# Kernel tuning notes

Measured on AMD Instinct MI355X. Metric: run time of the kernel, lower is better.

The kernel has to match this reference:

```python
import jax, jax.numpy as jnp
import numpy as np
import math

B, H, T, N = 2, 16, 4096, 64  # N = mlp_internal_dim_multiplier * n_embd // n_head = 1*1024//16
THETA = 2.0 ** 16


def _cos_sin(T, N):
    # quantized-theta RoPE tables, matching get_freqs + angle construction
    t = jnp.arange(N, dtype=jnp.float32)
    tq = jnp.floor(t / 2.0) * 2.0                      # quantize(t, q=2)
    freqs = 1.0 / (THETA ** (tq / N)) / (2.0 * math.pi)  # [N]
    phases = jnp.arange(T, dtype=jnp.float32)[:, None] * freqs[None, :]  # [T,N]
    ang = (phases % 1.0) * (2.0 * math.pi)
    return jnp.cos(ang), jnp.sin(ang)                  # each [T,N]


def setup_inputs() -> dict:
    key = jax.random.key(0)
    kq, kv = jax.random.split(key)
    Q = jax.random.normal(kq, (B, H, T, N), dtype=jnp.float32)
    V = jax.random.normal(kv, (B, H, T, N), dtype=jnp.float32)
    return {"Q": Q, "V": V}


def reference(Q, V):
    # K is Q (asserted in the torch module); RoPE applied to Q only.
    b, h, t, n = Q.shape
    cos, sin = _cos_sin(t, n)                          # [t,n], broadcast over b,h
    q_rot = jnp.stack((-Q[..., 1::2], Q[..., ::2]), axis=-1).reshape(Q.shape)
    QR = Q * cos + q_rot * sin                         # [b,h,t,n]
    scores = jnp.einsum('bhtn,bhsn->bhts', QR, QR) * (n ** -0.5)
    # strict lower-triangular mask (tril with diagonal=-1): no softmax
    mask = jnp.tril(jnp.ones((t, t), dtype=bool), k=-1)
    scores = jnp.where(mask, scores, 0.0)
    return jnp.einsum('bhts,bhsn->bhtn', scores, V)
```

## Files before the change

kernel.cpp:

```cpp
#include <hip/hip_runtime.h>

#define T_SEQ 4096
#define NDIM 64
#define BH 32
#define TN (T_SEQ * NDIM)

typedef short short8 __attribute__((ext_vector_type(8)));
typedef float f32x16 __attribute__((ext_vector_type(16)));

static __device__ __forceinline__ unsigned short f2bf(float x) {
    union { float f; unsigned u; } v; v.f = x;
    return (unsigned short)((v.u + 0x8000u) >> 16);
}

static __device__ __forceinline__ f32x16 mfma32(short8 a, short8 b, f32x16 c) {
    return __builtin_amdgcn_mfma_f32_32x32x16_bf16(a, b, c, 0, 0, 0);
}


__global__ __launch_bounds__(256) void rope_kernel(const float* __restrict__ Q,
                                                   unsigned short* __restrict__ qf) {
    const int bhtb = blockIdx.x;
    const int tb = bhtb & 127;
    const int bh = bhtb >> 7;
    const int np = threadIdx.x & 31;
    const int tg = threadIdx.x >> 5;
    const float freq = exp2f(-0.5f * (float)np) * 0.15915494309189535f;
    const int kc = np >> 3, hi = (np >> 2) & 1, jw = np & 3;
    const float2* qsrc = (const float2*)(Q + ((size_t)bh * T_SEQ + tb * 32) * NDIM);
    unsigned* qdst = (unsigned*)(qf + (size_t)bh * TN + (size_t)tb * 32 * NDIM);
#pragma unroll
    for (int it = 0; it < 4; ++it) {
        const int tl = tg * 4 + it;
        const int t = tb * 32 + tl;
        float2 q = qsrc[tl * 32 + np];
        float ph = (float)t * freq;
        float ang = (ph - floorf(ph)) * 6.283185307179586f;
        float s, c;
        __sincosf(ang, &s, &c);
        float r0 = q.x * c - q.y * s;
        float r1 = q.y * c + q.x * s;
        unsigned pk = (unsigned)f2bf(r0) | ((unsigned)f2bf(r1) << 16);
        qdst[kc * 256 + (tl * 2 + hi) * 4 + jw] = pk;
    }
}

__global__ __launch_bounds__(256) void vtrans_kernel(const float* __restrict__ V,
                                                     unsigned short* __restrict__ vfr) {
    __shared__ float tile[128 * 65];
    const int sb = blockIdx.x;
    const int bh = blockIdx.y;
    const int tid = threadIdx.x;
    const float* vsrc = V + ((size_t)bh * T_SEQ + sb * 128) * NDIM;
#pragma unroll
    for (int i = 0; i < 8; ++i) {
        int e = (i * 256 + tid) * 4;
        int row = e >> 6, col = e & 63;
        float4 d4 = *(const float4*)(vsrc + e);
        tile[row * 65 + col + 0] = d4.x; tile[row * 65 + col + 1] = d4.y;
        tile[row * 65 + col + 2] = d4.z; tile[row * 65 + col + 3] = d4.w;
    }
    __syncthreads();
    unsigned short* dst = vfr + (size_t)bh * TN + (size_t)sb * 8192;
#pragma unroll
    for (int u = 0; u < 4; ++u) {
        int g = u * 256 + tid;
        int kc = g >> 7, dh = g & 127;
        int d = dh >> 1, hh = dh & 1;
        int sbase = kc * 16 + hh * 8;
        ushort4 o0, o1;
        o0.x = f2bf(tile[(sbase + 0) * 65 + d] * 0.125f);
        o0.y = f2bf(tile[(sbase + 1) * 65 + d] * 0.125f);
        o0.z = f2bf(tile[(sbase + 2) * 65 + d] * 0.125f);
        o0.w = f2bf(tile[(sbase + 3) * 65 + d] * 0.125f);
        o1.x = f2bf(tile[(sbase + 4) * 65 + d] * 0.125f);
        o1.y = f2bf(tile[(sbase + 5) * 65 + d] * 0.125f);
        o1.z = f2bf(tile[(sbase + 6) * 65 + d] * 0.125f);
        o1.w = f2bf(tile[(sbase + 7) * 65 + d] * 0.125f);
        *(ushort4*)(dst + g * 8 + 0) = o0;
        *(ushort4*)(dst + g * 8 + 4) = o1;
    }
}

#define LDP 136

__global__ __launch_bounds__(256, 2) void attn_kernel(const unsigned short* __restrict__ qf,
                                                      const unsigned short* __restrict__ vfr,
                                                      float* __restrict__ out) {
    __shared__ unsigned short ps[128 * LDP];

    const int tid = threadIdx.x;
    const int lane = tid & 63;
    const int w = tid >> 6;
    const int ws = w >> 1, wt = w & 1;
    const int l31 = lane & 31, hi = lane >> 5;
    const int swz = (l31 & 8);

    const int blk = blockIdx.x;
    const int bh = blk & 31;
    const int qb = 31 - (blk >> 5);
    const int t0 = qb * 128;

    const unsigned short* qfh = qf + (size_t)bh * TN;
    const unsigned short* vfh = vfr + (size_t)bh * TN;
    float* out_h = out + (size_t)bh * TN;

    const int lhx16 = (l31 * 2 + hi) * 8;

    short8 bq[2][4];
#pragma unroll
    for (int tt2 = 0; tt2 < 2; ++tt2) {
        const int r32 = (t0 >> 5) + 2 * wt + tt2;
#pragma unroll
        for (int kc = 0; kc < 4; ++kc)
            bq[tt2][kc] = *(const short8*)(qfh + (size_t)(r32 * 4 + kc) * 512 + lhx16);
    }

    f32x16 oacc[2];
#pragma unroll
    for (int m = 0; m < 2; ++m)
#pragma unroll
        for (int r = 0; r < 16; ++r) oacc[m][r] = 0.0f;

    short8 ak[2][4];
#pragma unroll
    for (int st2 = 0; st2 < 2; ++st2) {
        const int r32 = 2 * ws + st2;
#pragma unroll
        for (int kc = 0; kc < 4; ++kc)
            ak[st2][kc] = *(const short8*)(qfh + (size_t)(r32 * 4 + kc) * 512 + lhx16);
    }

    for (int sb = 0; sb <= qb; ++sb) {
        short8 vf[8];
#pragma unroll
        for (int kc = 0; kc < 8; ++kc)
            vf[kc] = *(const short8*)(vfh + (size_t)sb * 8192 + (size_t)kc * 1024 +
                                      (size_t)wt * 512 + lhx16);

        f32x16 sacc[2][2];
#pragma unroll
        for (int a = 0; a < 2; ++a)
#pragma unroll
            for (int b = 0; b < 2; ++b)
#pragma unroll
                for (int r = 0; r < 16; ++r) sacc[a][b][r] = 0.0f;
#pragma unroll
        for (int st2 = 0; st2 < 2; ++st2)
#pragma unroll
            for (int tt2 = 0; tt2 < 2; ++tt2)
#pragma unroll
                for (int kc = 0; kc < 4; ++kc)
                    sacc[st2][tt2] = mfma32(ak[st2][kc], bq[tt2][kc], sacc[st2][tt2]);

        short8 akn[2][4];
        if (sb < qb) {
#pragma unroll
            for (int st2 = 0; st2 < 2; ++st2) {
                const int r32 = ((sb + 1) * 4) + 2 * ws + st2;
#pragma unroll
                for (int kc = 0; kc < 4; ++kc)
                    akn[st2][kc] = *(const short8*)(qfh + (size_t)(r32 * 4 + kc) * 512 + lhx16);
            }
        }

        __syncthreads();

        const bool diag = (sb == qb);
#pragma unroll
        for (int st2 = 0; st2 < 2; ++st2) {
            const int st = 2 * ws + st2;
#pragma unroll
            for (int tt2 = 0; tt2 < 2; ++tt2) {
                const int trow = (2 * wt + tt2) * 32 + l31;
                unsigned short* pbase = &ps[trow * LDP + st * 32 + 4 * hi + swz];
                if (!diag) {
#pragma unroll
                    for (int g = 0; g < 4; ++g) {
                        ushort4 pk;
                        pk.x = f2bf(sacc[st2][tt2][4 * g + 0]);
                        pk.y = f2bf(sacc[st2][tt2][4 * g + 1]);
                        pk.z = f2bf(sacc[st2][tt2][4 * g + 2]);
                        pk.w = f2bf(sacc[st2][tt2][4 * g + 3]);
                        *(ushort4*)(pbase + 8 * g) = pk;
                    }
                } else {
#pragma unroll
                    for (int g = 0; g < 4; ++g) {
                        ushort4 pk;
#pragma unroll
                        for (int e = 0; e < 4; ++e) {
                            const int srow = st * 32 + 8 * g + 4 * hi + e;
                            float v = sacc[st2][tt2][4 * g + e];
                            if (srow >= trow) v = 0.0f;
                            ((unsigned short*)&pk)[e] = f2bf(v);
                        }
                        *(ushort4*)(pbase + 8 * g) = pk;
                    }
                }
            }
        }
        __syncthreads();

#pragma unroll
        for (int kc = 0; kc < 8; ++kc) {
            short8 pf0 = *(const short8*)&ps[((2 * ws + 0) * 32 + l31) * LDP +
                                             kc * 16 + hi * 8 + swz];
            short8 pf1 = *(const short8*)&ps[((2 * ws + 1) * 32 + l31) * LDP +
                                             kc * 16 + hi * 8 + swz];
            oacc[0] = mfma32(pf0, vf[kc], oacc[0]);
            oacc[1] = mfma32(pf1, vf[kc], oacc[1]);
        }

        if (sb < qb) {
#pragma unroll
            for (int st2 = 0; st2 < 2; ++st2)
#pragma unroll
                for (int kc = 0; kc < 4; ++kc)
                    ak[st2][kc] = akn[st2][kc];
        }
    }

#pragma unroll
    for (int mt2 = 0; mt2 < 2; ++mt2) {
        const int mt = 2 * ws + mt2;
#pragma unroll
        for (int r = 0; r < 16; ++r) {
            const int rl = (r & 3) + 8 * (r >> 2) + 4 * hi;
            out_h[(size_t)(t0 + mt * 32 + rl) * NDIM + wt * 32 + l31] = oacc[mt2][r];
        }
    }
}

extern "C" void kernel_launch(void* const* d_in, const int* in_sizes, int n_in,
                              void* d_out, int out_size, void* d_ws, size_t ws_size,
                              hipStream_t stream) {
    (void)in_sizes; (void)n_in; (void)out_size; (void)ws_size;
    const float* Q = (const float*)d_in[0];
    const float* V = (const float*)d_in[1];
    float* out = (float*)d_out;

    unsigned short* qf  = (unsigned short*)d_ws;
    unsigned short* vfr = qf + (size_t)BH * TN;

    rope_kernel<<<BH * 128, 256, 0, stream>>>(Q, qf);
    vtrans_kernel<<<dim3(T_SEQ / 128, BH), 256, 0, stream>>>(V, vfr);
    attn_kernel<<<BH * 32, 256, 0, stream>>>(qf, vfr, out);
}
```

Measured before the change: 181.0 us.

## Keep score tiles in registers via permlane swap instead of LDS round-trip

The attention inner loop no longer writes bf16 score tiles to shared memory and reads them back with two barriers per block. The score accumulator is converted in registers into MFMA A-operand fragments using a cross-half lane swap (permlane32_swap or a bpermute fallback). The work split changes so each wave pair covers a slice of the key dimension and produces partial outputs. These partials are reduced once through LDS at the end. This removes per-iteration LDS traffic and synchronization, at the cost of more accumulator registers and a final cross-wave reduction.

```diff
diff --git a/kernel.cpp b/kernel.cpp
--- a/kernel.cpp
+++ b/kernel.cpp
@@ -7,16 +7,50 @@
 
 typedef short short8 __attribute__((ext_vector_type(8)));
 typedef float f32x16 __attribute__((ext_vector_type(16)));
+typedef unsigned uint2e __attribute__((ext_vector_type(2)));
 
 static __device__ __forceinline__ unsigned short f2bf(float x) {
     union { float f; unsigned u; } v; v.f = x;
     return (unsigned short)((v.u + 0x8000u) >> 16);
 }
-
+static __device__ __forceinline__ unsigned packbf(float lo, float hi) {
+    return (unsigned)f2bf(lo) | ((unsigned)f2bf(hi) << 16);
+}
 static __device__ __forceinline__ f32x16 mfma32(short8 a, short8 b, f32x16 c) {
     return __builtin_amdgcn_mfma_f32_32x32x16_bf16(a, b, c, 0, 0, 0);
 }
 
+static __device__ __forceinline__ void half_swap(unsigned &x, unsigned &y) {
+#if __has_builtin(__builtin_amdgcn_permlane32_swap)
+    uint2e r = __builtin_amdgcn_permlane32_swap(x, y, false, false);
+    x = r[0]; y = r[1];
+#else
+    int sl = (((int)threadIdx.x & 63) ^ 32) << 2;
+    unsigned bx = (unsigned)__builtin_amdgcn_ds_bpermute(sl, (int)x);
+    unsigned by = (unsigned)__builtin_amdgcn_ds_bpermute(sl, (int)y);
+    bool hi = (threadIdx.x & 32) != 0;
+    unsigned nx = hi ? by : x;
+    unsigned ny = hi ? y : bx;
+    x = nx; y = ny;
+#endif
+}
+
+static __device__ __forceinline__ void tile_to_frags(const f32x16 &sc, short8 &f0, short8 &f1) {
+    unsigned d[4][2];
+#pragma unroll
+    for (int g = 0; g < 4; ++g) {
+        d[g][0] = packbf(sc[4 * g + 0], sc[4 * g + 1]);
+        d[g][1] = packbf(sc[4 * g + 2], sc[4 * g + 3]);
+    }
+    half_swap(d[0][0], d[1][0]);
+    half_swap(d[0][1], d[1][1]);
+    half_swap(d[2][0], d[3][0]);
+    half_swap(d[2][1], d[3][1]);
+    union { unsigned u[4]; short8 s; } a, b;
+    a.u[0] = d[0][0]; a.u[1] = d[0][1]; a.u[2] = d[1][0]; a.u[3] = d[1][1];
+    b.u[0] = d[2][0]; b.u[1] = d[2][1]; b.u[2] = d[3][0]; b.u[3] = d[3][1];
+    f0 = a.s; f1 = b.s;
+}
 
 __global__ __launch_bounds__(256) void rope_kernel(const float* __restrict__ Q,
                                                    unsigned short* __restrict__ qf) {
@@ -82,19 +116,16 @@
     }
 }
 
-#define LDP 136
-
 __global__ __launch_bounds__(256, 2) void attn_kernel(const unsigned short* __restrict__ qf,
                                                       const unsigned short* __restrict__ vfr,
                                                       float* __restrict__ out) {
-    __shared__ unsigned short ps[128 * LDP];
+    __shared__ float4 red[2][4][4][64];
 
     const int tid = threadIdx.x;
     const int lane = tid & 63;
     const int w = tid >> 6;
     const int ws = w >> 1, wt = w & 1;
     const int l31 = lane & 31, hi = lane >> 5;
-    const int swz = (l31 & 8);
 
     const int blk = blockIdx.x;
     const int bh = blk & 31;
@@ -116,11 +147,13 @@
             bq[tt2][kc] = *(const short8*)(qfh + (size_t)(r32 * 4 + kc) * 512 + lhx16);
     }
 
-    f32x16 oacc[2];
-#pragma unroll
-    for (int m = 0; m < 2; ++m)
-#pragma unroll
-        for (int r = 0; r < 16; ++r) oacc[m][r] = 0.0f;
+    f32x16 oacc[2][2];
+#pragma unroll
+    for (int a = 0; a < 2; ++a)
+#pragma unroll
+        for (int b = 0; b < 2; ++b)
+#pragma unroll
+            for (int r = 0; r < 16; ++r) oacc[a][b][r] = 0.0f;
 
     short8 ak[2][4];
 #pragma unroll
@@ -132,12 +165,6 @@
     }
 
     for (int sb = 0; sb <= qb; ++sb) {
-        short8 vf[8];
-#pragma unroll
-        for (int kc = 0; kc < 8; ++kc)
-            vf[kc] = *(const short8*)(vfh + (size_t)sb * 8192 + (size_t)kc * 1024 +
-                                      (size_t)wt * 512 + lhx16);
-
         f32x16 sacc[2][2];
 #pragma unroll
         for (int a = 0; a < 2; ++a)
@@ -157,59 +184,45 @@
         if (sb < qb) {
 #pragma unroll
             for (int st2 = 0; st2 < 2; ++st2) {
-                const int r32 = ((sb + 1) * 4) + 2 * ws + st2;
+                const int r32 = (sb + 1) * 4 + 2 * ws + st2;
 #pragma unroll
                 for (int kc = 0; kc < 4; ++kc)
                     akn[st2][kc] = *(const short8*)(qfh + (size_t)(r32 * 4 + kc) * 512 + lhx16);
             }
         }
 
-        __syncthreads();
-
-        const bool diag = (sb == qb);
-#pragma unroll
-        for (int st2 = 0; st2 < 2; ++st2) {
-            const int st = 2 * ws + st2;
-#pragma unroll
-            for (int tt2 = 0; tt2 < 2; ++tt2) {
-                const int trow = (2 * wt + tt2) * 32 + l31;
-                unsigned short* pbase = &ps[trow * LDP + st * 32 + 4 * hi + swz];
-                if (!diag) {
-#pragma unroll
-                    for (int g = 0; g < 4; ++g) {
-                        ushort4 pk;
-                        pk.x = f2bf(sacc[st2][tt2][4 * g + 0]);
-                        pk.y = f2bf(sacc[st2][tt2][4 * g + 1]);
-                        pk.z = f2bf(sacc[st2][tt2][4 * g + 2]);
-                        pk.w = f2bf(sacc[st2][tt2][4 * g + 3]);
-                        *(ushort4*)(pbase + 8 * g) = pk;
+        if (sb == qb) {
+#pragma unroll
+            for (int st2 = 0; st2 < 2; ++st2) {
+                const int st = 2 * ws + st2;
+#pragma unroll
+                for (int tt2 = 0; tt2 < 2; ++tt2) {
+                    const int tg = (2 * wt + tt2) * 32 + l31;
+#pragma unroll
+                    for (int r = 0; r < 16; ++r) {
+                        const int sg = st * 32 + (r & 3) + 8 * (r >> 2) + 4 * hi;
+                        if (sg >= tg) sacc[st2][tt2][r] = 0.0f;
                     }
-                } else {
-#pragma unroll
-                    for (int g = 0; g < 4; ++g) {
-                        ushort4 pk;
-#pragma unroll
-                        for (int e = 0; e < 4; ++e) {
-                            const int srow = st * 32 + 8 * g + 4 * hi + e;
-                            float v = sacc[st2][tt2][4 * g + e];
-                            if (srow >= trow) v = 0.0f;
-                            ((unsigned short*)&pk)[e] = f2bf(v);
-                        }
-                        *(ushort4*)(pbase + 8 * g) = pk;
-                    }
                 }
             }
         }
-        __syncthreads();
-
-#pragma unroll
-        for (int kc = 0; kc < 8; ++kc) {
-            short8 pf0 = *(const short8*)&ps[((2 * ws + 0) * 32 + l31) * LDP +
-                                             kc * 16 + hi * 8 + swz];
-            short8 pf1 = *(const short8*)&ps[((2 * ws + 1) * 32 + l31) * LDP +
-                                             kc * 16 + hi * 8 + swz];
-            oacc[0] = mfma32(pf0, vf[kc], oacc[0]);
-            oacc[1] = mfma32(pf1, vf[kc], oacc[1]);
+
+        short8 pa[2][4];
+#pragma unroll
+        for (int st2 = 0; st2 < 2; ++st2)
+#pragma unroll
+            for (int tt2 = 0; tt2 < 2; ++tt2)
+                tile_to_frags(sacc[st2][tt2], pa[tt2][2 * st2 + 0], pa[tt2][2 * st2 + 1]);
+
+#pragma unroll
+        for (int kc4 = 0; kc4 < 4; ++kc4) {
+            const int kcg = 4 * ws + kc4;
+            short8 v0 = *(const short8*)(vfh + (size_t)sb * 8192 + (size_t)kcg * 1024 + lhx16);
+            short8 v1 = *(const short8*)(vfh + (size_t)sb * 8192 + (size_t)kcg * 1024 + 512 + lhx16);
+            oacc[0][0] = mfma32(pa[0][kc4], v0, oacc[0][0]);
+            oacc[0][1] = mfma32(pa[0][kc4], v1, oacc[0][1]);
+            oacc[1][0] = mfma32(pa[1][kc4], v0, oacc[1][0]);
+            oacc[1][1] = mfma32(pa[1][kc4], v1, oacc[1][1]);
         }
 
         if (sb < qb) {
@@ -221,14 +234,42 @@
         }
     }
 
-#pragma unroll
-    for (int mt2 = 0; mt2 < 2; ++mt2) {
-        const int mt = 2 * ws + mt2;
-#pragma unroll
-        for (int r = 0; r < 16; ++r) {
-            const int rl = (r & 3) + 8 * (r >> 2) + 4 * hi;
-            out_h[(size_t)(t0 + mt * 32 + rl) * NDIM + wt * 32 + l31] = oacc[mt2][r];
-        }
+    if (ws == 1) {
+#pragma unroll
+        for (int tt2 = 0; tt2 < 2; ++tt2)
+#pragma unroll
+            for (int dd = 0; dd < 2; ++dd)
+#pragma unroll
+                for (int g = 0; g < 4; ++g) {
+                    float4 v;
+                    v.x = oacc[tt2][dd][4 * g + 0];
+                    v.y = oacc[tt2][dd][4 * g + 1];
+                    v.z = oacc[tt2][dd][4 * g + 2];
+                    v.w = oacc[tt2][dd][4 * g + 3];
+                    red[wt][tt2 * 2 + dd][g][lane] = v;
+                }
+    }
+    __syncthreads();
+    if (ws == 0) {
+#pragma unroll
+        for (int tt2 = 0; tt2 < 2; ++tt2)
+#pragma unroll
+            for (int dd = 0; dd < 2; ++dd) {
+#pragma unroll
+                for (int g = 0; g < 4; ++g) {
+                    float4 o = red[wt][tt2 * 2 + dd][g][lane];
+                    oacc[tt2][dd][4 * g + 0] += o.x;
+                    oacc[tt2][dd][4 * g + 1] += o.y;
+                    oacc[tt2][dd][4 * g + 2] += o.z;
+                    oacc[tt2][dd][4 * g + 3] += o.w;
+                }
+#pragma unroll
+                for (int r = 0; r < 16; ++r) {
+                    const int rl = (r & 3) + 8 * (r >> 2) + 4 * hi;
+                    out_h[(size_t)(t0 + 64 * wt + 32 * tt2 + rl) * NDIM + 32 * dd + l31] =
+                        oacc[tt2][dd][r];
+                }
+            }
     }
 }
 
```

Result: slower. 186.8 us (+3.2%).
